# Performance work log

Measured on AMD Instinct MI355X. Metric: run time of the kernel, lower is better.

Reference implementation:

```python
import jax, jax.numpy as jnp
import numpy as np

N = 100000   # nodes
C = 128      # channels
K = 16       # clusters
E = 3200000  # edges (avg degree 32)


def setup_inputs() -> dict:
    key = jax.random.key(0)
    k1, k2, k3, k4 = jax.random.split(key, 4)
    features = jax.random.normal(k1, (N, C), dtype=jnp.float32)
    edge_row = jax.random.randint(k2, (E,), 0, N, dtype=jnp.int32)
    edge_col = jax.random.randint(k3, (E,), 0, N, dtype=jnp.int32)
    edge_val = jnp.ones((E,), dtype=jnp.float32)
    # orthogonal-ish init for fc weight (matches nn.init.orthogonal_ in spirit)
    w = jax.random.normal(k4, (K, C), dtype=jnp.float32)
    q, _ = jnp.linalg.qr(w.T)          # [C, K], orthonormal columns
    fc_w = q.T.astype(jnp.float32)     # [K, C]
    fc_b = jnp.zeros((K,), dtype=jnp.float32)
    return {"features": features, "edge_row": edge_row, "edge_col": edge_col,
            "edge_val": edge_val, "fc_w": fc_w, "fc_b": fc_b}


def reference(features, edge_row, edge_col, edge_val, fc_w, fc_b):
    collapse_regularization = 1.0
    n_nodes = features.shape[0]
    n_clusters = fc_w.shape[0]

    # assignments = softmax(Linear(features))  -> [N, K]
    assignments = jax.nn.softmax(features @ fc_w.T + fc_b, axis=1)
    cluster_sizes = jnp.sum(assignments, axis=0)            # [K]
    assignments_pooling = assignments / cluster_sizes       # [N, K]

    # degrees = column sums of sparse adjacency (no densification)
    degrees = jax.ops.segment_sum(edge_val, edge_col, num_segments=n_nodes)  # [N]
    number_of_edges = jnp.sum(degrees)

    # sparse A @ assignments via segment_sum over edges -> [N, K]
    a_s = jax.ops.segment_sum(edge_val[:, None] * assignments[edge_col],
                              edge_row, num_segments=n_nodes)
    graph_pooled = a_s.T @ assignments                      # S^T A S, [K, K]

    normalizer_left = assignments.T @ degrees[:, None]      # [K, 1]
    normalizer_right = degrees[None, :] @ assignments       # [1, K]
    normalizer = (normalizer_left @ normalizer_right) / 2.0 / number_of_edges

    spectral_loss = -jnp.trace(graph_pooled - normalizer) / 2.0 / number_of_edges
    sk = np.sqrt(n_clusters).astype(np.float32)
    collapse_loss = (jnp.sum(jnp.abs(cluster_sizes - n_nodes / n_clusters))
                     / n_nodes * sk / (sk - 1.0) / 2.0)
    loss = spectral_loss + collapse_regularization * collapse_loss

    features_pooled = jax.nn.selu(assignments_pooling.T @ features)  # [K, C]
    features_pooled = assignments_pooling @ features_pooled          # unpool [N, C]
    return features_pooled, assignments, loss
```

## Files before the change

### kernel.cpp

```cpp
#include <hip/hip_runtime.h>
#include <math.h>


#define WS_ESUM 0
#define WS_TR   1
#define WS_M    2
#define WS_CS   18
#define WS_B    64
#define WS_P2   2112
#define WS_PART 4160

__global__ __launch_bounds__(256) void k_assign(
    const float* __restrict__ F, const float* __restrict__ W,
    const float* __restrict__ bias, float* __restrict__ A,
    float* __restrict__ csp, int N) {
  __shared__ float Ws[2048];
  __shared__ float csred[4][16];
  int t = threadIdx.x;
#pragma unroll
  for (int i = 0; i < 8; i++) Ws[t + 256 * i] = W[t + 256 * i];
  __syncthreads();

  int n = blockIdx.x * 256 + t;
  float a[16];
  if (n < N) {
#pragma unroll
    for (int k = 0; k < 16; k++) a[k] = bias[k];
    const float4* f4 = (const float4*)(F + (size_t)n * 128);
#pragma unroll 4
    for (int i = 0; i < 32; i++) {
      float4 f = f4[i];
#pragma unroll
      for (int k = 0; k < 16; k++) {
        float4 w = *(const float4*)(&Ws[k * 128 + i * 4]);
        a[k] = fmaf(f.x, w.x, a[k]);
        a[k] = fmaf(f.y, w.y, a[k]);
        a[k] = fmaf(f.z, w.z, a[k]);
        a[k] = fmaf(f.w, w.w, a[k]);
      }
    }
    float mx = a[0];
#pragma unroll
    for (int k = 1; k < 16; k++) mx = fmaxf(mx, a[k]);
    float s = 0.f;
#pragma unroll
    for (int k = 0; k < 16; k++) { a[k] = __expf(a[k] - mx); s += a[k]; }
    float inv = 1.0f / s;
#pragma unroll
    for (int k = 0; k < 16; k++) a[k] *= inv;
    float4* o = (float4*)(A + (size_t)n * 16);
    o[0] = make_float4(a[0], a[1], a[2], a[3]);
    o[1] = make_float4(a[4], a[5], a[6], a[7]);
    o[2] = make_float4(a[8], a[9], a[10], a[11]);
    o[3] = make_float4(a[12], a[13], a[14], a[15]);
  } else {
#pragma unroll
    for (int k = 0; k < 16; k++) a[k] = 0.f;
  }

#pragma unroll
  for (int k = 0; k < 16; k++) {
    float v = a[k];
    for (int off = 32; off; off >>= 1) v += __shfl_xor(v, off, 64);
    a[k] = v;
  }
  int lane = t & 63, wid = t >> 6;
  if (lane == 0) {
#pragma unroll
    for (int k = 0; k < 16; k++) csred[wid][k] = a[k];
  }
  __syncthreads();
  if (t < 16)
    csp[(size_t)blockIdx.x * 16 + t] =
        csred[0][t] + csred[1][t] + csred[2][t] + csred[3][t];
}

__global__ __launch_bounds__(256) void k_edge(
    const int* __restrict__ row, const int* __restrict__ col,
    const float* __restrict__ val, const float* __restrict__ A,
    float* __restrict__ ep, int E) {
  float eS = 0.f, tr = 0.f;
  float m[16];
#pragma unroll
  for (int i = 0; i < 16; i++) m[i] = 0.f;

  int tid = blockIdx.x * 256 + threadIdx.x;
  int T = gridDim.x * 256;
  for (int e = tid; e < E; e += T) {
    int r = row[e], c = col[e];
    float v = val[e];
    const float4* Ac4 = (const float4*)(A + (size_t)c * 16);
    const float4* Ar4 = (const float4*)(A + (size_t)r * 16);
    float4 c0 = Ac4[0], c1 = Ac4[1], c2 = Ac4[2], c3 = Ac4[3];
    float4 r0 = Ar4[0], r1 = Ar4[1], r2 = Ar4[2], r3 = Ar4[3];
    eS += v;
    m[0]  = fmaf(v, c0.x, m[0]);  m[1]  = fmaf(v, c0.y, m[1]);
    m[2]  = fmaf(v, c0.z, m[2]);  m[3]  = fmaf(v, c0.w, m[3]);
    m[4]  = fmaf(v, c1.x, m[4]);  m[5]  = fmaf(v, c1.y, m[5]);
    m[6]  = fmaf(v, c1.z, m[6]);  m[7]  = fmaf(v, c1.w, m[7]);
    m[8]  = fmaf(v, c2.x, m[8]);  m[9]  = fmaf(v, c2.y, m[9]);
    m[10] = fmaf(v, c2.z, m[10]); m[11] = fmaf(v, c2.w, m[11]);
    m[12] = fmaf(v, c3.x, m[12]); m[13] = fmaf(v, c3.y, m[13]);
    m[14] = fmaf(v, c3.z, m[14]); m[15] = fmaf(v, c3.w, m[15]);
    float d = r0.x * c0.x + r0.y * c0.y + r0.z * c0.z + r0.w * c0.w
            + r1.x * c1.x + r1.y * c1.y + r1.z * c1.z + r1.w * c1.w
            + r2.x * c2.x + r2.y * c2.y + r2.z * c2.z + r2.w * c2.w
            + r3.x * c3.x + r3.y * c3.y + r3.z * c3.z + r3.w * c3.w;
    tr = fmaf(v, d, tr);
  }

  float vals[18];
  vals[0] = eS; vals[1] = tr;
#pragma unroll
  for (int i = 0; i < 16; i++) vals[2 + i] = m[i];
#pragma unroll
  for (int i = 0; i < 18; i++) {
    float v = vals[i];
    for (int off = 32; off; off >>= 1) v += __shfl_xor(v, off, 64);
    vals[i] = v;
  }
  __shared__ float red[4][18];
  int lane = threadIdx.x & 63, wid = threadIdx.x >> 6;
  if (lane == 0) {
#pragma unroll
    for (int i = 0; i < 18; i++) red[wid][i] = vals[i];
  }
  __syncthreads();
  if (threadIdx.x < 18)
    ep[(size_t)blockIdx.x * 18 + threadIdx.x] =
        red[0][threadIdx.x] + red[1][threadIdx.x] +
        red[2][threadIdx.x] + red[3][threadIdx.x];
}

__global__ __launch_bounds__(256) void k_nodeB(
    const float* __restrict__ F, const float* __restrict__ A,
    float* __restrict__ bp, int N) {
  int t = threadIdx.x;
  int q = t & 31;
  int sub = t >> 5;

  float4 acc[16];
#pragma unroll
  for (int k = 0; k < 16; k++) acc[k] = make_float4(0.f, 0.f, 0.f, 0.f);

  const float4* F4 = (const float4*)F;
  const float4* A4 = (const float4*)A;
  int stride = gridDim.x * 8;
  for (int n = blockIdx.x * 8 + sub; n < N; n += stride) {
    float4 f  = F4[(size_t)n * 32 + q];
    float4 a0 = A4[(size_t)n * 4 + 0];
    float4 a1 = A4[(size_t)n * 4 + 1];
    float4 a2 = A4[(size_t)n * 4 + 2];
    float4 a3 = A4[(size_t)n * 4 + 3];
    float av[16] = {a0.x, a0.y, a0.z, a0.w, a1.x, a1.y, a1.z, a1.w,
                    a2.x, a2.y, a2.z, a2.w, a3.x, a3.y, a3.z, a3.w};
#pragma unroll
    for (int k = 0; k < 16; k++) {
      acc[k].x = fmaf(av[k], f.x, acc[k].x);
      acc[k].y = fmaf(av[k], f.y, acc[k].y);
      acc[k].z = fmaf(av[k], f.z, acc[k].z);
      acc[k].w = fmaf(av[k], f.w, acc[k].w);
    }
  }

#pragma unroll
  for (int k = 0; k < 16; k++) {
    acc[k].x += __shfl_xor(acc[k].x, 32, 64);
    acc[k].y += __shfl_xor(acc[k].y, 32, 64);
    acc[k].z += __shfl_xor(acc[k].z, 32, 64);
    acc[k].w += __shfl_xor(acc[k].w, 32, 64);
  }

  __shared__ float red[4][2048];
  int lane = t & 63, wid = t >> 6;
  if (lane < 32) {
#pragma unroll
    for (int k = 0; k < 16; k++)
      *(float4*)&red[wid][k * 128 + q * 4] = acc[k];
  }
  __syncthreads();
  float* myp = bp + (size_t)blockIdx.x * 2048;
#pragma unroll
  for (int qq = 0; qq < 2; qq++) {
    int base = t * 8 + qq * 4;
    float4 s0 = *(float4*)&red[0][base];
    float4 s1 = *(float4*)&red[1][base];
    float4 s2 = *(float4*)&red[2][base];
    float4 s3 = *(float4*)&red[3][base];
    *(float4*)&myp[base] = make_float4(s0.x + s1.x + s2.x + s3.x,
                                       s0.y + s1.y + s2.y + s3.y,
                                       s0.z + s1.z + s2.z + s3.z,
                                       s0.w + s1.w + s2.w + s3.w);
  }
}

__global__ __launch_bounds__(256) void k_reduce(
    const float* __restrict__ csp, const float* __restrict__ ep,
    const float* __restrict__ bp, float* __restrict__ ws,
    int GA, int GE, int GB) {
  __shared__ float L[256];
  int t = threadIdx.x;
  int b = blockIdx.x;
  if (b < 32) {
    int cell = b * 64 + (t & 63);
    int seg = t >> 6;
    float s = 0.f;
    for (int g = seg; g < GB; g += 4) s += bp[(size_t)g * 2048 + cell];
    L[t] = s;
    __syncthreads();
    if (t < 64)
      ws[WS_B + b * 64 + t] = L[t] + L[64 + t] + L[128 + t] + L[192 + t];
  } else if (b == 32) {
    int i = t % 18, s = t / 18;
    float v = 0.f;
    if (s < 14) {
      for (int g = s; g < GE; g += 14) v += ep[(size_t)g * 18 + i];
    }
    L[t] = v;
    __syncthreads();
    if (t < 18) {
      float tot = 0.f;
#pragma unroll
      for (int ss = 0; ss < 14; ss++) tot += L[ss * 18 + t];
      ws[t] = tot;
    }
  } else {
    int i = t & 15, s = t >> 4;
    float v = 0.f;
    for (int g = s; g < GA; g += 16) v += csp[(size_t)g * 16 + i];
    L[t] = v;
    __syncthreads();
    if (t < 16) {
      float tot = 0.f;
#pragma unroll
      for (int ss = 0; ss < 16; ss++) tot += L[ss * 16 + t];
      ws[WS_CS + t] = tot;
    }
  }
}

__global__ __launch_bounds__(256) void k_finalize(
    float* __restrict__ ws, float* __restrict__ loss_out, int N) {
  __shared__ float invcs[16];
  int t = threadIdx.x;
  if (t < 16) invcs[t] = 1.0f / ws[WS_CS + t];
  __syncthreads();
  const float* B = ws + WS_B;
  float* P2 = ws + WS_P2;
  const float scale = 1.0507009873554805f;
  const float alpha = 1.6732632423543772f;
#pragma unroll
  for (int idx = t; idx < 2048; idx += 256) {
    int k = idx >> 7;
    float x = B[idx] * invcs[k];
    float s = (x > 0.f) ? scale * x : scale * alpha * expm1f(x);
    P2[idx] = s * invcs[k];
  }
  if (t == 0) {
    float Es = ws[WS_ESUM], tr = ws[WS_TR];
    float m2 = 0.f;
#pragma unroll
    for (int i = 0; i < 16; i++) m2 += ws[WS_M + i] * ws[WS_M + i];
    float spectral = -(tr - m2 / (2.0f * Es)) / (2.0f * Es);
    float coll = 0.f;
    float tgt = (float)N / 16.0f;
#pragma unroll
    for (int i = 0; i < 16; i++) coll += fabsf(ws[WS_CS + i] - tgt);
    coll = coll / (float)N * (4.0f / 3.0f / 2.0f);
    loss_out[0] = spectral + coll;
  }
}

__global__ __launch_bounds__(256) void k_unpool(
    const float* __restrict__ A, const float* __restrict__ P2,
    float* __restrict__ out, int N) {
  __shared__ float Ps[2048];
  int t = threadIdx.x;
#pragma unroll
  for (int i = 0; i < 8; i++) Ps[t + 256 * i] = P2[t + 256 * i];
  __syncthreads();
  int c = t & 127;
  int half = t >> 7;
  int pairs = (N + 1) >> 1;
  for (int p = blockIdx.x; p < pairs; p += gridDim.x) {
    int n = p * 2 + half;
    if (n < N) {
      const float4* a4 = (const float4*)(A + (size_t)n * 16);
      float4 a0 = a4[0], a1 = a4[1], a2 = a4[2], a3 = a4[3];
      float s = a0.x * Ps[0 * 128 + c] + a0.y * Ps[1 * 128 + c]
              + a0.z * Ps[2 * 128 + c] + a0.w * Ps[3 * 128 + c]
              + a1.x * Ps[4 * 128 + c] + a1.y * Ps[5 * 128 + c]
              + a1.z * Ps[6 * 128 + c] + a1.w * Ps[7 * 128 + c]
              + a2.x * Ps[8 * 128 + c] + a2.y * Ps[9 * 128 + c]
              + a2.z * Ps[10 * 128 + c] + a2.w * Ps[11 * 128 + c]
              + a3.x * Ps[12 * 128 + c] + a3.y * Ps[13 * 128 + c]
              + a3.z * Ps[14 * 128 + c] + a3.w * Ps[15 * 128 + c];
      out[(size_t)n * 128 + c] = s;
    }
  }
}

extern "C" void kernel_launch(void* const* d_in, const int* in_sizes, int n_in,
                              void* d_out, int out_size, void* d_ws, size_t ws_size,
                              hipStream_t stream) {
  const float* F    = (const float*)d_in[0];
  const int*   erow = (const int*)d_in[1];
  const int*   ecol = (const int*)d_in[2];
  const float* eval_= (const float*)d_in[3];
  const float* W    = (const float*)d_in[4];
  const float* bias = (const float*)d_in[5];

  int N = in_sizes[0] / 128;
  int E = in_sizes[1];

  float* out0 = (float*)d_out;
  float* A    = out0 + (size_t)N * 128;
  float* loss = A + (size_t)N * 16;
  float* ws   = (float*)d_ws;

  int GA = (N + 255) / 256;
  int GE = 1024;
  int GB = 256;

  size_t availf = ws_size / 4;
  size_t off_csp = WS_PART;
  size_t off_ep  = off_csp + (size_t)GA * 16;
  size_t need = off_ep + (size_t)GE * 18 + (size_t)GB * 2048;
  while (need > availf && GB > 1) { GB >>= 1; need = off_ep + (size_t)GE * 18 + (size_t)GB * 2048; }
  while (need > availf && GE > 1) { GE >>= 1; need = off_ep + (size_t)GE * 18 + (size_t)GB * 2048; }
  size_t off_bp = off_ep + (size_t)GE * 18;

  float* csp = ws + off_csp;
  float* ep  = ws + off_ep;
  float* bp  = ws + off_bp;

  k_assign<<<GA, 256, 0, stream>>>(F, W, bias, A, csp, N);
  k_edge<<<GE, 256, 0, stream>>>(erow, ecol, eval_, A, ep, E);
  k_nodeB<<<GB, 256, 0, stream>>>(F, A, bp, N);
  k_reduce<<<34, 256, 0, stream>>>(csp, ep, bp, ws, GA, GE, GB);
  k_finalize<<<1, 256, 0, stream>>>(ws, loss, N);
  k_unpool<<<1024, 256, 0, stream>>>(A, ws + WS_P2, out0, N);
}
```

Measured before the change: 278.4 us.

## Gather fp16 assignment copy in edge kernel and split assign rows across lanes

The assignment kernel now gives each node to four lanes, each doing a quarter of the 128-channel dot product, combines the partials with shuffles, and writes an extra fp16 copy of the assignments. The edge kernel gathers that half-precision copy, halving the bytes per random row/col gather, and widens to fp32 before accumulating. Scratch buffers (fp16 copy, partials) are now placed inside the not-yet-written output region instead of the workspace, and GB is raised to 1024. This risks precision loss in the trace term and depends on k_unpool overwriting that scratch only after it has been consumed.

```diff
diff --git a/kernel.cpp b/kernel.cpp
--- a/kernel.cpp
+++ b/kernel.cpp
@@ -1,4 +1,5 @@
 #include <hip/hip_runtime.h>
+#include <hip/hip_fp16.h>
 #include <math.h>
 
 
@@ -8,12 +9,16 @@
 #define WS_CS   18
 #define WS_B    64
 #define WS_P2   2112
-#define WS_PART 4160
+
+#define OFF_AH  0
+#define OFF_CSP 800000
+#define OFF_EP  825008
+#define OFF_BP  843440
 
 __global__ __launch_bounds__(256) void k_assign(
     const float* __restrict__ F, const float* __restrict__ W,
     const float* __restrict__ bias, float* __restrict__ A,
-    float* __restrict__ csp, int N) {
+    __half* __restrict__ Ah, float* __restrict__ csp, int N) {
   __shared__ float Ws[2048];
   __shared__ float csred[4][16];
   int t = threadIdx.x;
@@ -21,53 +26,75 @@
   for (int i = 0; i < 8; i++) Ws[t + 256 * i] = W[t + 256 * i];
   __syncthreads();
 
-  int n = blockIdx.x * 256 + t;
+  int p = t & 3;
+  int nl = t >> 2;
+  int n = blockIdx.x * 64 + nl;
+  bool active = (n < N);
+
   float a[16];
-  if (n < N) {
-#pragma unroll
-    for (int k = 0; k < 16; k++) a[k] = bias[k];
-    const float4* f4 = (const float4*)(F + (size_t)n * 128);
-#pragma unroll 4
-    for (int i = 0; i < 32; i++) {
+#pragma unroll
+  for (int k = 0; k < 16; k++) a[k] = 0.f;
+
+  if (active) {
+    const float4* f4 = (const float4*)(F + (size_t)n * 128 + p * 32);
+#pragma unroll
+    for (int i = 0; i < 8; i++) {
       float4 f = f4[i];
 #pragma unroll
       for (int k = 0; k < 16; k++) {
-        float4 w = *(const float4*)(&Ws[k * 128 + i * 4]);
+        float4 w = *(const float4*)(&Ws[k * 128 + p * 32 + i * 4]);
         a[k] = fmaf(f.x, w.x, a[k]);
         a[k] = fmaf(f.y, w.y, a[k]);
         a[k] = fmaf(f.z, w.z, a[k]);
         a[k] = fmaf(f.w, w.w, a[k]);
       }
     }
-    float mx = a[0];
-#pragma unroll
-    for (int k = 1; k < 16; k++) mx = fmaxf(mx, a[k]);
-    float s = 0.f;
-#pragma unroll
-    for (int k = 0; k < 16; k++) { a[k] = __expf(a[k] - mx); s += a[k]; }
-    float inv = 1.0f / s;
-#pragma unroll
-    for (int k = 0; k < 16; k++) a[k] *= inv;
-    float4* o = (float4*)(A + (size_t)n * 16);
-    o[0] = make_float4(a[0], a[1], a[2], a[3]);
-    o[1] = make_float4(a[4], a[5], a[6], a[7]);
-    o[2] = make_float4(a[8], a[9], a[10], a[11]);
-    o[3] = make_float4(a[12], a[13], a[14], a[15]);
-  } else {
-#pragma unroll
-    for (int k = 0; k < 16; k++) a[k] = 0.f;
   }
 
 #pragma unroll
   for (int k = 0; k < 16; k++) {
-    float v = a[k];
+    a[k] += __shfl_xor(a[k], 1, 64);
+    a[k] += __shfl_xor(a[k], 2, 64);
+  }
+
+#pragma unroll
+  for (int k = 0; k < 16; k++) a[k] += bias[k];
+  float mx = a[0];
+#pragma unroll
+  for (int k = 1; k < 16; k++) mx = fmaxf(mx, a[k]);
+  float s = 0.f;
+#pragma unroll
+  for (int k = 0; k < 16; k++) { a[k] = __expf(a[k] - mx); s += a[k]; }
+  float inv = 1.0f / s;
+#pragma unroll
+  for (int k = 0; k < 16; k++) a[k] *= inv;
+
+  if (active) {
+    float4 g = make_float4(a[p * 4 + 0], a[p * 4 + 1], a[p * 4 + 2], a[p * 4 + 3]);
+    ((float4*)(A + (size_t)n * 16))[p] = g;
+    if (p == 0) {
+      __half2 hh[4];
+      hh[0].x = __float2half_rn(a[0]); hh[0].y = __float2half_rn(a[1]);
+      hh[1].x = __float2half_rn(a[2]); hh[1].y = __float2half_rn(a[3]);
+      hh[2].x = __float2half_rn(a[4]); hh[2].y = __float2half_rn(a[5]);
+      hh[3].x = __float2half_rn(a[6]); hh[3].y = __float2half_rn(a[7]);
+      *(uint4*)(Ah + (size_t)n * 16) = *(uint4*)hh;
+    } else if (p == 1) {
+      __half2 hh[4];
+      hh[0].x = __float2half_rn(a[8]);  hh[0].y = __float2half_rn(a[9]);
+      hh[1].x = __float2half_rn(a[10]); hh[1].y = __float2half_rn(a[11]);
+      hh[2].x = __float2half_rn(a[12]); hh[2].y = __float2half_rn(a[13]);
+      hh[3].x = __float2half_rn(a[14]); hh[3].y = __float2half_rn(a[15]);
+      *(uint4*)(Ah + (size_t)n * 16 + 8) = *(uint4*)hh;
+    }
+  }
+
+  int lane = t & 63, wid = t >> 6;
+#pragma unroll
+  for (int k = 0; k < 16; k++) {
+    float v = (active && p == 0) ? a[k] : 0.f;
     for (int off = 32; off; off >>= 1) v += __shfl_xor(v, off, 64);
-    a[k] = v;
-  }
-  int lane = t & 63, wid = t >> 6;
-  if (lane == 0) {
-#pragma unroll
-    for (int k = 0; k < 16; k++) csred[wid][k] = a[k];
+    if (lane == 0) csred[wid][k] = v;
   }
   __syncthreads();
   if (t < 16)
@@ -75,9 +102,11 @@
         csred[0][t] + csred[1][t] + csred[2][t] + csred[3][t];
 }
 
+union H2F4 { float4 f4; __half2 h2[4]; };
+
 __global__ __launch_bounds__(256) void k_edge(
     const int* __restrict__ row, const int* __restrict__ col,
-    const float* __restrict__ val, const float* __restrict__ A,
+    const float* __restrict__ val, const __half* __restrict__ Ah,
     float* __restrict__ ep, int E) {
   float eS = 0.f, tr = 0.f;
   float m[16];
@@ -89,23 +118,27 @@
   for (int e = tid; e < E; e += T) {
     int r = row[e], c = col[e];
     float v = val[e];
-    const float4* Ac4 = (const float4*)(A + (size_t)c * 16);
-    const float4* Ar4 = (const float4*)(A + (size_t)r * 16);
-    float4 c0 = Ac4[0], c1 = Ac4[1], c2 = Ac4[2], c3 = Ac4[3];
-    float4 r0 = Ar4[0], r1 = Ar4[1], r2 = Ar4[2], r3 = Ar4[3];
+    const float4* pc = (const float4*)(Ah + (size_t)c * 16);
+    const float4* pr = (const float4*)(Ah + (size_t)r * 16);
+    H2F4 uc0, uc1, ur0, ur1;
+    uc0.f4 = pc[0]; uc1.f4 = pc[1];
+    ur0.f4 = pr[0]; ur1.f4 = pr[1];
+    float cf[16], rf[16];
+#pragma unroll
+    for (int j = 0; j < 4; j++) {
+      float2 f;
+      f = __half22float2(uc0.h2[j]); cf[2 * j] = f.x; cf[2 * j + 1] = f.y;
+      f = __half22float2(uc1.h2[j]); cf[8 + 2 * j] = f.x; cf[9 + 2 * j] = f.y;
+      f = __half22float2(ur0.h2[j]); rf[2 * j] = f.x; rf[2 * j + 1] = f.y;
+      f = __half22float2(ur1.h2[j]); rf[8 + 2 * j] = f.x; rf[9 + 2 * j] = f.y;
+    }
     eS += v;
-    m[0]  = fmaf(v, c0.x, m[0]);  m[1]  = fmaf(v, c0.y, m[1]);
-    m[2]  = fmaf(v, c0.z, m[2]);  m[3]  = fmaf(v, c0.w, m[3]);
-    m[4]  = fmaf(v, c1.x, m[4]);  m[5]  = fmaf(v, c1.y, m[5]);
-    m[6]  = fmaf(v, c1.z, m[6]);  m[7]  = fmaf(v, c1.w, m[7]);
-    m[8]  = fmaf(v, c2.x, m[8]);  m[9]  = fmaf(v, c2.y, m[9]);
-    m[10] = fmaf(v, c2.z, m[10]); m[11] = fmaf(v, c2.w, m[11]);
-    m[12] = fmaf(v, c3.x, m[12]); m[13] = fmaf(v, c3.y, m[13]);
-    m[14] = fmaf(v, c3.z, m[14]); m[15] = fmaf(v, c3.w, m[15]);
-    float d = r0.x * c0.x + r0.y * c0.y + r0.z * c0.z + r0.w * c0.w
-            + r1.x * c1.x + r1.y * c1.y + r1.z * c1.z + r1.w * c1.w
-            + r2.x * c2.x + r2.y * c2.y + r2.z * c2.z + r2.w * c2.w
-            + r3.x * c3.x + r3.y * c3.y + r3.z * c3.z + r3.w * c3.w;
+    float d = 0.f;
+#pragma unroll
+    for (int k = 0; k < 16; k++) {
+      m[k] = fmaf(v, cf[k], m[k]);
+      d = fmaf(rf[k], cf[k], d);
+    }
     tr = fmaf(v, d, tr);
   }
 
@@ -318,24 +351,17 @@
   float* loss = A + (size_t)N * 16;
   float* ws   = (float*)d_ws;
 
-  int GA = (N + 255) / 256;
+  int GA = (N + 63) / 64;
   int GE = 1024;
-  int GB = 256;
-
-  size_t availf = ws_size / 4;
-  size_t off_csp = WS_PART;
-  size_t off_ep  = off_csp + (size_t)GA * 16;
-  size_t need = off_ep + (size_t)GE * 18 + (size_t)GB * 2048;
-  while (need > availf && GB > 1) { GB >>= 1; need = off_ep + (size_t)GE * 18 + (size_t)GB * 2048; }
-  while (need > availf && GE > 1) { GE >>= 1; need = off_ep + (size_t)GE * 18 + (size_t)GB * 2048; }
-  size_t off_bp = off_ep + (size_t)GE * 18;
-
-  float* csp = ws + off_csp;
-  float* ep  = ws + off_ep;
-  float* bp  = ws + off_bp;
-
-  k_assign<<<GA, 256, 0, stream>>>(F, W, bias, A, csp, N);
-  k_edge<<<GE, 256, 0, stream>>>(erow, ecol, eval_, A, ep, E);
+  int GB = 1024;
+
+  __half* Ah  = (__half*)(out0 + OFF_AH);
+  float*  csp = out0 + OFF_CSP;
+  float*  ep  = out0 + OFF_EP;
+  float*  bp  = out0 + OFF_BP;
+
+  k_assign<<<GA, 256, 0, stream>>>(F, W, bias, A, Ah, csp, N);
+  k_edge<<<GE, 256, 0, stream>>>(erow, ecol, eval_, Ah, ep, E);
   k_nodeB<<<GB, 256, 0, stream>>>(F, A, bp, N);
   k_reduce<<<34, 256, 0, stream>>>(csp, ep, bp, ws, GA, GE, GB);
   k_finalize<<<1, 256, 0, stream>>>(ws, loss, N);
```

Result: slower. 336.6 us (+20.9%).
